# Optimization experiments

Measured on AMD Instinct MI355X. Metric: run time of the kernel, lower is better.

Reference implementation:

```python
import jax, jax.numpy as jnp
import numpy as np

N_E, E_DIM, BETA = 8192, 512, 0.25


def setup_inputs() -> dict:
    key = jax.random.key(0)
    k1, k2 = jax.random.split(key)
    z = jax.random.normal(k1, (16, 1024, E_DIM), dtype=jnp.float32)
    # embedding initialized uniform(-1/n_e, 1/n_e)
    emb_w = jax.random.uniform(k2, (N_E, E_DIM), dtype=jnp.float32,
                               minval=-1.0 / N_E, maxval=1.0 / N_E)
    return {"z": z, "emb_w": emb_w}


def reference(z, emb_w):
    B, T, D = z.shape
    zf = z.reshape(-1, D)  # [BT, D]
    # squared-distance matrix: ||z||^2 + ||e||^2 - 2 z e^T  -> [BT, n_e]
    d = (jnp.sum(zf * zf, axis=1, keepdims=True)
         + jnp.sum(emb_w * emb_w, axis=1)
         - 2.0 * jnp.einsum('bd,nd->bn', zf, emb_w))
    idx = jnp.argmin(d, axis=1)  # [BT]
    z_q = emb_w[idx].reshape(z.shape)  # [B, T, D]
    # legacy=False: beta * commit + codebook term
    loss = (BETA * jnp.mean((jax.lax.stop_gradient(z_q) - z) ** 2)
            + jnp.mean((z_q - jax.lax.stop_gradient(z)) ** 2))
    # straight-through: value equals z_q
    z_q_st = z + jax.lax.stop_gradient(z_q - z)
    idx_out = idx.reshape(B, T)
    v = jnp.var(idx_out.astype(jnp.float32))
    return z_q_st, loss, idx_out, v
```

## Files before the change

### kernel.cpp

```cpp
#include <hip/hip_runtime.h>


#define BT   16384
#define DIMS 512
#define NE   8192
#define NS   4
#define BN   256
#define NTPB (NE / NS / BN)
#define NSTEPS 64

#define LOSS_OFF 8388608
#define IDX_OFF  8388609
#define V_OFF    8404993

#define BEST_OFF  0
#define ENORM_OFF 131072
#define SUMS_OFF  163840
#define CNT_OFF   163864

typedef __attribute__((ext_vector_type(8))) short short8;
typedef __attribute__((ext_vector_type(4))) float floatx4;

#define AS1(p) ((const __attribute__((address_space(1))) void*)(p))
#define AS3(p) ((__attribute__((address_space(3))) void*)(p))

__device__ __forceinline__ unsigned f2bf(float f) {
    unsigned u = __builtin_bit_cast(unsigned, f);
    u += 0x7FFFu + ((u >> 16) & 1u);
    return u >> 16;
}

__global__ __launch_bounds__(256) void prep_kernel(
    const float* __restrict__ z, const float* __restrict__ emb,
    ushort* __restrict__ zh, ushort* __restrict__ ehh,
    float* __restrict__ enorm, unsigned long long* __restrict__ best,
    double* __restrict__ sums, unsigned* __restrict__ counter)
{
    const int lane = threadIdx.x & 63, w = threadIdx.x >> 6;
    const int b = blockIdx.x;
    if (b < NE / 4) {
        const int row = b * 4 + w;
        const float4* p = (const float4*)(emb + (size_t)row * DIMS + lane * 8);
        float4 a = p[0], bb = p[1];
        uint4 h;
        h.x = f2bf(a.x) | (f2bf(a.y) << 16);
        h.y = f2bf(a.z) | (f2bf(a.w) << 16);
        h.z = f2bf(bb.x) | (f2bf(bb.y) << 16);
        h.w = f2bf(bb.z) | (f2bf(bb.w) << 16);
        *(uint4*)(ehh + (size_t)row * DIMS + lane * 8) = h;
        float s = a.x*a.x + a.y*a.y + a.z*a.z + a.w*a.w
                + bb.x*bb.x + bb.y*bb.y + bb.z*bb.z + bb.w*bb.w;
        #pragma unroll
        for (int off = 32; off > 0; off >>= 1) s += __shfl_down(s, off, 64);
        if (lane == 0) enorm[row] = s;
    } else {
        const int row = (b - NE / 4) * 4 + w;
        const float4* p = (const float4*)(z + (size_t)row * DIMS + lane * 8);
        float4 a = p[0], bb = p[1];
        uint4 h;
        h.x = f2bf(a.x) | (f2bf(a.y) << 16);
        h.y = f2bf(a.z) | (f2bf(a.w) << 16);
        h.z = f2bf(bb.x) | (f2bf(bb.y) << 16);
        h.w = f2bf(bb.z) | (f2bf(bb.w) << 16);
        *(uint4*)(zh + (size_t)row * DIMS + lane * 8) = h;
    }
    const int gid = b * 256 + threadIdx.x;
    if (gid < BT) best[gid] = 0xFFFFFFFFFFFFFFFFULL;
    if (gid == 0) { sums[0] = 0.0; sums[1] = 0.0; sums[2] = 0.0; *counter = 0u; }
}


__device__ __forceinline__ void dsr_fence() {
    asm volatile("s_waitcnt lgkmcnt(0)" ::: "memory");
    __builtin_amdgcn_sched_barrier(0);
}

#define DSR8(dst, IDX) do {                                                    \
    unsigned a_ = (unsigned)(size_t)AS3(&lds[IDX]);                            \
    asm volatile("ds_read_b128 %0, %1" : "=v"(dst) : "v"(a_));                 \
} while (0)

#define PH_SYNC()                                                              \
    __builtin_amdgcn_sched_barrier(0);                                         \
    __builtin_amdgcn_s_barrier();                                              \
    dsr_fence();

#define MFMA16(KK, NJ0)                                                        \
    __builtin_amdgcn_s_setprio(1);                                             \
    _Pragma("unroll")                                                          \
    for (int j2 = 0; j2 < 4; j2++)                                             \
        _Pragma("unroll")                                                      \
        for (int mi = 0; mi < 4; mi++)                                         \
            acc[mi][(NJ0) + j2] = __builtin_amdgcn_mfma_f32_16x16x32_bf16(     \
                a[mi][KK], b[j2], acc[mi][(NJ0) + j2], 0, 0, 0);               \
    __builtin_amdgcn_s_setprio(0);

#define STAGE_A(SA_, H_) do {                                                  \
    const int sa_ = (SA_);                                                     \
    const int sc_ = sa_ & 63;                                                  \
    const unsigned al_ = (unsigned)(sa_ & 1) * 32768u                          \
                       + (unsigned)((((H_) * 128) + w * 8) * 64);              \
    const ushort* g_ = zA + (size_t)((H_) * 128) * DIMS + soff                 \
                     + ((sc_ & 7) * 64);                                       \
    __builtin_amdgcn_global_load_lds(AS1(g_), AS3(&lds[al_]), 16, 0, 0);       \
    __builtin_amdgcn_global_load_lds(AS1(g_ + (size_t)64 * DIMS),              \
                                     AS3(&lds[al_ + 64 * 64]), 16, 0, 0);      \
} while (0)

#define STAGE_B(SB_, H_) do {                                                  \
    const int sb_ = (SB_);                                                     \
    const int sc_ = sb_ & 63;                                                  \
    const unsigned bl_ = 16384u + (unsigned)(sb_ & 1) * 32768u                 \
                       + (unsigned)((((H_) * 128) + w * 8) * 64);              \
    const ushort* g_ = eh + (size_t)(nsN + (sc_ >> 3) * 256 + (H_) * 128) * DIMS \
                     + soff + ((sc_ & 7) * 64);                                \
    __builtin_amdgcn_global_load_lds(AS1(g_), AS3(&lds[bl_]), 16, 0, 0);       \
    __builtin_amdgcn_global_load_lds(AS1(g_ + (size_t)64 * DIMS),              \
                                     AS3(&lds[bl_ + 64 * 64]), 16, 0, 0);      \
} while (0)

#define STEP(S_, AB_, TM_) do {                                                \
    const int s_ = (S_);                                                       \
    short8 a[4][2], b[4];                                                      \
                      \
    _Pragma("unroll") for (int mi = 0; mi < 4; mi++)                           \
        DSR8(a[mi][0], (AB_) + aro + mi * 1024 + pxo0);                        \
    _Pragma("unroll") for (int j2 = 0; j2 < 4; j2++)                           \
        DSR8(b[j2], 16384u + (AB_) + bro + j2 * 1024 + pxo0);                  \
    STAGE_B(s_ + 1, 0);                                                        \
    PH_SYNC(); MFMA16(0, 0);                                                   \
    __builtin_amdgcn_s_barrier();                                              \
                      \
    _Pragma("unroll") for (int mi = 0; mi < 4; mi++)                           \
        DSR8(a[mi][1], (AB_) + aro + mi * 1024 + pxo1);                        \
    _Pragma("unroll") for (int j2 = 0; j2 < 4; j2++)                           \
        DSR8(b[j2], 16384u + (AB_) + bro + (4 + j2) * 1024 + pxo0);            \
    STAGE_B(s_ + 1, 1);                                                        \
    PH_SYNC(); MFMA16(0, 4);                                                   \
    __builtin_amdgcn_s_barrier();                                              \
          \
    _Pragma("unroll") for (int j2 = 0; j2 < 4; j2++)                           \
        DSR8(b[j2], 16384u + (AB_) + bro + j2 * 1024 + pxo1);                  \
    STAGE_A(s_ + 2, 0);                                                        \
    PH_SYNC(); MFMA16(1, 0);                                                   \
    __builtin_amdgcn_s_barrier();                                              \
        \
    _Pragma("unroll") for (int j2 = 0; j2 < 4; j2++)                           \
        DSR8(b[j2], 16384u + (AB_) + bro + (4 + j2) * 1024 + pxo1);            \
    STAGE_A(s_ + 2, 1);                                                        \
    PH_SYNC(); MFMA16(1, 4);                                                   \
    if ((TM_) == 0) asm volatile("s_waitcnt vmcnt(4)" ::: "memory");           \
    __builtin_amdgcn_s_barrier();                                              \
} while (0)

__global__ __launch_bounds__(512, 2) void argmin_mfma(
    const ushort* __restrict__ zh, const ushort* __restrict__ eh,
    const float* __restrict__ enorm, unsigned long long* __restrict__ best)
{
    __shared__ __align__(16) ushort lds[69632];
    float* elds = (float*)&lds[65536];

    const int t = threadIdx.x;
    const int w = t >> 6, lane = t & 63;
    const int quad = lane >> 4, l15 = lane & 15;

    const int d = blockIdx.x;
    const int xcd = d & 7, slot = d >> 3;
    const int ns = xcd >> 1;
    const int mt = slot * 2 + (xcd & 1);
    const int m0 = mt * 256;
    const int nsN = ns * (NTPB * BN);

    const int wrow = (w & 3) * 64;
    const int wcol = (w >> 2) * 128;

    {
        float4 v = *(const float4*)(enorm + nsN + t * 4);
        *(float4*)(elds + t * 4) = v;
    }
    __syncthreads();

    const int l8 = lane >> 3, c8 = lane & 7;
    const int chunk = c8 ^ l8;
    const int soff = (w * 8 + l8) * DIMS + chunk * 8;
    const ushort* zA = zh + (size_t)m0 * DIMS;

    const int pxo0 = (quad ^ (l15 & 7)) * 8;
    const int pxo1 = ((4 + quad) ^ (l15 & 7)) * 8;
    const int aro = (wrow + l15) * 64;
    const int bro = (wcol + l15) * 64;

    floatx4 acc[4][8];
    #pragma unroll
    for (int mi = 0; mi < 4; mi++)
        #pragma unroll
        for (int nj = 0; nj < 8; nj++)
            acc[mi][nj] = (floatx4){0.f, 0.f, 0.f, 0.f};

    float bs[16];
    int   bn_[16];
    #pragma unroll
    for (int k = 0; k < 16; k++) { bs[k] = 3.4e38f; bn_[k] = 0; }

    STAGE_A(0, 0); STAGE_A(0, 1);
    STAGE_B(0, 0); STAGE_B(0, 1);
    STAGE_A(1, 0); STAGE_A(1, 1);
    asm volatile("s_waitcnt vmcnt(4)" ::: "memory");
    __builtin_amdgcn_s_barrier();

    for (int sp = 0; sp < NSTEPS; sp += 2) {
        STEP(sp, 0u, 0);
        STEP(sp + 1, 32768u, (sp == NSTEPS - 2) ? 2 : 0);

        if ((sp & 7) == 6) {
            const int nt = sp >> 3;
            const int eb = nt * 256 + wcol + l15;
            const int nbase = nsN + eb;
            float en[8];
            #pragma unroll
            for (int nj = 0; nj < 8; nj++) {
                unsigned a_ = (unsigned)(size_t)AS3(&elds[eb + nj * 16]);
                asm volatile("ds_read_b32 %0, %1" : "=v"(en[nj]) : "v"(a_));
            }
            dsr_fence();
            #pragma unroll
            for (int nj = 0; nj < 8; nj++) {
                const int n = nbase + nj * 16;
                #pragma unroll
                for (int mi = 0; mi < 4; mi++) {
                    #pragma unroll
                    for (int r = 0; r < 4; r++) {
                        const int k = mi * 4 + r;
                        const float sc = fmaf(-2.0f, acc[mi][nj][r], en[nj]);
                        if (sc < bs[k]) { bs[k] = sc; bn_[k] = n; }
                    }
                    acc[mi][nj] = (floatx4){0.f, 0.f, 0.f, 0.f};
                }
            }
        }
    }

    #pragma unroll
    for (int mi = 0; mi < 4; mi++)
        #pragma unroll
        for (int r = 0; r < 4; r++) {
            const int k = mi * 4 + r;
            unsigned su = __builtin_bit_cast(unsigned, bs[k]);
            su = (su & 0x80000000u) ? ~su : (su | 0x80000000u);
            unsigned long long key = ((unsigned long long)su << 32) | (unsigned)bn_[k];
            #pragma unroll
            for (int off = 1; off < 16; off <<= 1) {
                unsigned long long o = __shfl_xor(key, off, 64);
                key = (o < key) ? o : key;
            }
            if (l15 == 0) atomicMin(&best[m0 + wrow + mi * 16 + quad * 4 + r], key);
        }
}

__global__ __launch_bounds__(256) void gather_loss_kernel(
    const float* __restrict__ z, const float* __restrict__ emb,
    const unsigned long long* __restrict__ best,
    float* __restrict__ out, double* __restrict__ sums, unsigned* __restrict__ counter)
{
    __shared__ int sIdx[32];
    __shared__ double red[4];
    const int t = threadIdx.x;
    const int row0 = blockIdx.x * 32;
    double myIdxSum = 0.0, myIdxSq = 0.0;
    if (t < 32) {
        int row = row0 + t;
        int idx = (int)(unsigned)(best[row] & 0xFFFFFFFFULL);
        sIdx[t] = idx;
        out[IDX_OFF + row] = (float)idx;
        myIdxSum = (double)idx;
        myIdxSq = (double)idx * (double)idx;
    }
    __syncthreads();
    double acc = 0.0;
    #pragma unroll 4
    for (int i = 0; i < 16; i++) {
        int e = i * 1024 + t * 4;
        int rl = e >> 9;
        int c = e & 511;
        int idx = sIdx[rl];
        float4 zv = *(const float4*)(z + (size_t)(row0 + rl) * DIMS + c);
        float4 ev = *(const float4*)(emb + (size_t)idx * DIMS + c);
        *(float4*)(out + (size_t)(row0 + rl) * DIMS + c) = ev;
        float dx = zv.x - ev.x, dy = zv.y - ev.y;
        float dz = zv.z - ev.z, dw = zv.w - ev.w;
        acc += (double)(dx * dx + dy * dy) + (double)(dz * dz + dw * dw);
    }
    const int lane = t & 63, wv = t >> 6;
    #pragma unroll
    for (int off = 32; off > 0; off >>= 1) {
        acc      += __shfl_down(acc, off, 64);
        myIdxSum += __shfl_down(myIdxSum, off, 64);
        myIdxSq  += __shfl_down(myIdxSq, off, 64);
    }
    if (lane == 0) red[wv] = acc;
    __syncthreads();
    if (t == 0) {
        double tot = red[0] + red[1] + red[2] + red[3];
        atomicAdd(&sums[0], tot);
        atomicAdd(&sums[1], myIdxSum);
        atomicAdd(&sums[2], myIdxSq);
        __threadfence();
        unsigned old = atomicAdd(counter, 1u);
        if (old == gridDim.x - 1) {
            __threadfence();
            double s0 = atomicAdd(&sums[0], 0.0);
            double s1 = atomicAdd(&sums[1], 0.0);
            double s2 = atomicAdd(&sums[2], 0.0);
            out[LOSS_OFF] = (float)(1.25 * s0 / (double)((size_t)BT * DIMS));
            double m = s1 / (double)BT;
            out[V_OFF] = (float)(s2 / (double)BT - m * m);
        }
    }
}

extern "C" void kernel_launch(void* const* d_in, const int* in_sizes, int n_in,
                              void* d_out, int out_size, void* d_ws, size_t ws_size,
                              hipStream_t stream) {
    const float* z = (const float*)d_in[0];
    const float* emb = (const float*)d_in[1];
    float* out = (float*)d_out;
    char* ws = (char*)d_ws;
    unsigned long long* best = (unsigned long long*)(ws + BEST_OFF);
    float* enorm  = (float*)(ws + ENORM_OFF);
    double* sums  = (double*)(ws + SUMS_OFF);
    unsigned* counter = (unsigned*)(ws + CNT_OFF);

    ushort* zh = (ushort*)out;
    ushort* ehh = zh + (size_t)BT * DIMS;

    hipLaunchKernelGGL(prep_kernel, dim3(NE / 4 + BT / 4), dim3(256), 0, stream,
                       z, emb, zh, ehh, enorm, best, sums, counter);
    hipLaunchKernelGGL(argmin_mfma, dim3(256), dim3(512), 0, stream,
                       zh, ehh, enorm, best);
    hipLaunchKernelGGL(gather_loss_kernel, dim3(BT / 32), dim3(256), 0, stream,
                       z, emb, best, out, sums, counter);
}
```

Measured before the change: 258.0 us.

## Halve per-step barriers and interleave MFMAs with fine-grained LDS waits

Reworks the inner GEMM step of the argmin kernel from four barrier-separated phases to two barriers per step. It loads more B fragments into registers and issues MFMA groups behind staged s_waitcnt lgkmcnt waits, so each group starts as soon as its operands arrive instead of after a full LDS drain. The two A-staging global-to-LDS loads now run together after a barrier that guards reuse of the current A buffer, and a final vmcnt(0) wait is added before the epilogue. This cuts workgroup synchronization and LDS-latency stalls, at the cost of higher register pressure from eight B fragments and a tighter ordering dependency for buffer reuse.

```diff
diff --git a/kernel.cpp b/kernel.cpp
--- a/kernel.cpp
+++ b/kernel.cpp
@@ -76,24 +76,20 @@
 }
 
 #define DSR8(dst, IDX) do {                                                    \
-    unsigned a_ = (unsigned)(size_t)AS3(&lds[IDX]);                            \
-    asm volatile("ds_read_b128 %0, %1" : "=v"(dst) : "v"(a_));                 \
-} while (0)
-
-#define PH_SYNC()                                                              \
+    unsigned addr_ = (unsigned)(size_t)AS3(&lds[IDX]);                         \
+    asm volatile("ds_read_b128 %0, %1" : "=v"(dst) : "v"(addr_));              \
+} while (0)
+
+#define LGK(N_) do {                                                           \
+    asm volatile("s_waitcnt lgkmcnt(" #N_ ")" ::: "memory");                   \
     __builtin_amdgcn_sched_barrier(0);                                         \
-    __builtin_amdgcn_s_barrier();                                              \
-    dsr_fence();
-
-#define MFMA16(KK, NJ0)                                                        \
-    __builtin_amdgcn_s_setprio(1);                                             \
+} while (0)
+
+#define CL4(J_, BIDX_)                                                         \
     _Pragma("unroll")                                                          \
-    for (int j2 = 0; j2 < 4; j2++)                                             \
-        _Pragma("unroll")                                                      \
-        for (int mi = 0; mi < 4; mi++)                                         \
-            acc[mi][(NJ0) + j2] = __builtin_amdgcn_mfma_f32_16x16x32_bf16(     \
-                a[mi][KK], b[j2], acc[mi][(NJ0) + j2], 0, 0, 0);               \
-    __builtin_amdgcn_s_setprio(0);
+    for (int mi = 0; mi < 4; mi++)                                             \
+        acc[mi][J_] = __builtin_amdgcn_mfma_f32_16x16x32_bf16(                 \
+            a[mi], b[BIDX_], acc[mi][J_], 0, 0, 0);
 
 #define STAGE_A(SA_, H_) do {                                                  \
     const int sa_ = (SA_);                                                     \
@@ -121,34 +117,41 @@
 
 #define STEP(S_, AB_, TM_) do {                                                \
     const int s_ = (S_);                                                       \
-    short8 a[4][2], b[4];                                                      \
-                      \
+    short8 a[4], b[8];                                                         \
+                                                                       \
     _Pragma("unroll") for (int mi = 0; mi < 4; mi++)                           \
-        DSR8(a[mi][0], (AB_) + aro + mi * 1024 + pxo0);                        \
-    _Pragma("unroll") for (int j2 = 0; j2 < 4; j2++)                           \
-        DSR8(b[j2], 16384u + (AB_) + bro + j2 * 1024 + pxo0);                  \
+        DSR8(a[mi], (AB_) + aro + mi * 1024 + pxo0);                           \
+    _Pragma("unroll") for (int j = 0; j < 4; j++)                              \
+        DSR8(b[j], 16384u + (AB_) + bro + j * 1024 + pxo0);                    \
     STAGE_B(s_ + 1, 0);                                                        \
-    PH_SYNC(); MFMA16(0, 0);                                                   \
-    __builtin_amdgcn_s_barrier();                                              \
-                      \
+    __builtin_amdgcn_s_setprio(1);                                             \
+    LGK(3); CL4(0, 0); LGK(2); CL4(1, 1); LGK(1); CL4(2, 2); LGK(0); CL4(3, 3);\
+    __builtin_amdgcn_s_setprio(0);                                             \
+                                                                       \
+    _Pragma("unroll") for (int j = 0; j < 4; j++)                              \
+        DSR8(b[4 + j], 16384u + (AB_) + bro + (4 + j) * 1024 + pxo0);          \
+    _Pragma("unroll") for (int j = 0; j < 4; j++)                              \
+        DSR8(b[j], 16384u + (AB_) + bro + j * 1024 + pxo1);                    \
+    STAGE_B(s_ + 1, 1);                                                        \
+    __builtin_amdgcn_s_setprio(1);                                             \
+    LGK(7); CL4(4, 4); LGK(6); CL4(5, 5); LGK(5); CL4(6, 6); LGK(4); CL4(7, 7);\
+    __builtin_amdgcn_s_setprio(0);                                             \
+                                                                       \
     _Pragma("unroll") for (int mi = 0; mi < 4; mi++)                           \
-        DSR8(a[mi][1], (AB_) + aro + mi * 1024 + pxo1);                        \
-    _Pragma("unroll") for (int j2 = 0; j2 < 4; j2++)                           \
-        DSR8(b[j2], 16384u + (AB_) + bro + (4 + j2) * 1024 + pxo0);            \
-    STAGE_B(s_ + 1, 1);                                                        \
-    PH_SYNC(); MFMA16(0, 4);                                                   \
-    __builtin_amdgcn_s_barrier();                                              \
-          \
-    _Pragma("unroll") for (int j2 = 0; j2 < 4; j2++)                           \
-        DSR8(b[j2], 16384u + (AB_) + bro + j2 * 1024 + pxo1);                  \
-    STAGE_A(s_ + 2, 0);                                                        \
-    PH_SYNC(); MFMA16(1, 0);                                                   \
-    __builtin_amdgcn_s_barrier();                                              \
-        \
-    _Pragma("unroll") for (int j2 = 0; j2 < 4; j2++)                           \
-        DSR8(b[j2], 16384u + (AB_) + bro + (4 + j2) * 1024 + pxo1);            \
-    STAGE_A(s_ + 2, 1);                                                        \
-    PH_SYNC(); MFMA16(1, 4);                                                   \
+        DSR8(a[mi], (AB_) + aro + mi * 1024 + pxo1);                           \
+    _Pragma("unroll") for (int j = 0; j < 4; j++)                              \
+        DSR8(b[4 + j], 16384u + (AB_) + bro + (4 + j) * 1024 + pxo1);          \
+    __builtin_amdgcn_s_setprio(1);                                             \
+    LGK(4); CL4(0, 0); CL4(1, 1); CL4(2, 2); CL4(3, 3);                        \
+    __builtin_amdgcn_s_setprio(0);                                             \
+    __builtin_amdgcn_sched_barrier(0);                                         \
+    __builtin_amdgcn_s_barrier();            \
+                                                                       \
+    STAGE_A(s_ + 2, 0); STAGE_A(s_ + 2, 1);                                    \
+    __builtin_amdgcn_s_setprio(1);                                             \
+    LGK(3); CL4(4, 4); LGK(2); CL4(5, 5); LGK(1); CL4(6, 6); LGK(0); CL4(7, 7);\
+    __builtin_amdgcn_s_setprio(0);                                             \
+    __builtin_amdgcn_sched_barrier(0);                                         \
     if ((TM_) == 0) asm volatile("s_waitcnt vmcnt(4)" ::: "memory");           \
     __builtin_amdgcn_s_barrier();                                              \
 } while (0)
@@ -219,8 +222,8 @@
             float en[8];
             #pragma unroll
             for (int nj = 0; nj < 8; nj++) {
-                unsigned a_ = (unsigned)(size_t)AS3(&elds[eb + nj * 16]);
-                asm volatile("ds_read_b32 %0, %1" : "=v"(en[nj]) : "v"(a_));
+                unsigned addr_ = (unsigned)(size_t)AS3(&elds[eb + nj * 16]);
+                asm volatile("ds_read_b32 %0, %1" : "=v"(en[nj]) : "v"(addr_));
             }
             dsr_fence();
             #pragma unroll
@@ -239,6 +242,8 @@
             }
         }
     }
+
+    asm volatile("s_waitcnt vmcnt(0)" ::: "memory");
 
     #pragma unroll
     for (int mi = 0; mi < 4; mi++)
```

After: 244.2 us. -5.3%, faster.
